# Kernel tuning notes

Hardware: AMD Instinct MI355X
Metric: run time of the kernel (lower is better)

Reference implementation:

```python
import jax, jax.numpy as jnp
import numpy as np

B, N, D, H, K = 8, 10000, 128, 4, 256
DH = D // H
M = N // 2


def make_pe(n, d):
    pos = jnp.arange(n, dtype=jnp.float32)[:, None]
    div = jnp.exp(jnp.arange(0, d, 2, dtype=jnp.float32) * (-jnp.log(10000.0) / d))
    ang = pos * div  # [n, d/2]
    pe = jnp.zeros((n, d), dtype=jnp.float32)
    pe = pe.at[:, 0::2].set(jnp.sin(ang))
    pe = pe.at[:, 1::2].set(jnp.cos(ang))
    return pe


def layernorm(z, g, b, eps=1e-5):
    mu = jnp.mean(z, -1, keepdims=True)
    var = jnp.var(z, -1, keepdims=True)
    return (z - mu) / jnp.sqrt(var + eps) * g + b


def setup_inputs():
    key = jax.random.key(0)
    ks = jax.random.split(key, 12)
    def rn(k, shape, scale):
        return jax.random.normal(k, shape, dtype=jnp.float32) * scale
    return {
        "x": rn(ks[0], (B, N), 1.0),
        "emb_w": rn(ks[1], (D, 1), 0.5),
        "emb_b": rn(ks[2], (D,), 0.02),
        "ln1_g": jnp.ones((D,), jnp.float32),
        "ln1_b": jnp.zeros((D,), jnp.float32),
        "wq": rn(ks[3], (D, D), D ** -0.5),
        "wk": rn(ks[4], (D, D), D ** -0.5),
        "wv": rn(ks[5], (D, D), D ** -0.5),
        "proj_k": rn(ks[6], (N, K), N ** -0.5),
        "proj_v": rn(ks[7], (N, K), N ** -0.5),
        "wo": rn(ks[8], (D, D), D ** -0.5),
        "wo_b": jnp.zeros((D,), jnp.float32),
        "ln2_g": jnp.ones((D,), jnp.float32),
        "ln2_b": jnp.zeros((D,), jnp.float32),
        "w1": rn(ks[9], (4 * D, D), D ** -0.5),
        "b1": jnp.zeros((4 * D,), jnp.float32),
        "w2": rn(ks[10], (D, 4 * D), (4 * D) ** -0.5),
        "b2": jnp.zeros((D,), jnp.float32),
        "fc_w": rn(ks[11], (M, N), N ** -0.5),
        "fc_b": jnp.zeros((M,), jnp.float32),
    }


def reference(x, emb_w, emb_b, ln1_g, ln1_b, wq, wk, wv, proj_k, proj_v, wo, wo_b,
              ln2_g, ln2_b, w1, b1, w2, b2, fc_w, fc_b):
    b, n = x.shape
    # Linear embedding of scalar per position: [B,N] -> [B,N,D]
    xe = x[..., None] @ emb_w.T + emb_b
    xe = xe + make_pe(n, D)
    # --- Linformer self-attention block (pre-norm + residual) ---
    hn = layernorm(xe, ln1_g, ln1_b)
    q = hn @ wq.T                                        # [B,N,D]
    k = jnp.einsum('bnd,nk->bkd', hn @ wk.T, proj_k)     # low-rank keys   [B,K,D]
    v = jnp.einsum('bnd,nk->bkd', hn @ wv.T, proj_v)     # low-rank values [B,K,D]
    q = q.reshape(b, n, H, DH).transpose(0, 2, 1, 3)     # [B,H,N,DH]
    k = k.reshape(b, K, H, DH).transpose(0, 2, 1, 3)     # [B,H,K,DH]
    v = v.reshape(b, K, H, DH).transpose(0, 2, 1, 3)
    attn = jax.nn.softmax(jnp.einsum('bhnd,bhkd->bhnk', q, k) * (DH ** -0.5), axis=-1)
    out = jnp.einsum('bhnk,bhkd->bhnd', attn, v).transpose(0, 2, 1, 3).reshape(b, n, D)
    xe = xe + out @ wo.T + wo_b
    # --- FeedForward block (pre-norm + residual, exact GELU) ---
    hn = layernorm(xe, ln2_g, ln2_b)
    xe = xe + (jax.nn.gelu(hn @ w1.T + b1, approximate=False) @ w2.T + b2)
    # fc over seq dim (Linear(N, N//2) applied to [B,D,N]) then sum-pool over D
    y = jnp.einsum('bnd,mn->bdm', xe, fc_w) + fc_b       # [B,D,M]
    return jnp.sum(y, axis=1)                            # [B,M]
```

## Files before the change

### kernel.cpp

```cpp
#include <hip/hip_runtime.h>

constexpr int B_ = 8, N_ = 10000, D_ = 128, H_ = 4, K_ = 256, M_ = 5000, DFF_ = 512;
constexpr int NPAD = 10240;

typedef __attribute__((ext_vector_type(8))) short bf16x8;
typedef __attribute__((ext_vector_type(4))) float f32x4;

__device__ __forceinline__ float bf2f(unsigned short u) {
    unsigned x = ((unsigned)u) << 16; float f; __builtin_memcpy(&f, &x, 4); return f;
}
__device__ __forceinline__ unsigned short f2bf(float f) {
    unsigned x; __builtin_memcpy(&x, &f, 4);
    x = (x + 0x7fffu + ((x >> 16) & 1u)) >> 16;
    return (unsigned short)x;
}
__device__ __forceinline__ unsigned pack2(float a, float b) {
    return (unsigned)f2bf(a) | ((unsigned)f2bf(b) << 16);
}
__device__ __forceinline__ float gelu_exact(float v) {
    return 0.5f * v * (1.0f + erff(v * 0.70710678118654752f));
}

__global__ __launch_bounds__(256) void cvt_w_k(
    const float* __restrict__ s0, const float* __restrict__ s1, const float* __restrict__ s2,
    const float* __restrict__ s3, const float* __restrict__ s4, const float* __restrict__ s5,
    unsigned short* __restrict__ d0, unsigned short* __restrict__ d1, unsigned short* __restrict__ d2,
    unsigned short* __restrict__ d3, unsigned short* __restrict__ d4, unsigned short* __restrict__ d5)
{
    const float* s; unsigned short* d; int sz;
    switch (blockIdx.y) {
        case 0: s = s0; d = d0; sz = 16384; break;
        case 1: s = s1; d = d1; sz = 16384; break;
        case 2: s = s2; d = d2; sz = 16384; break;
        case 3: s = s3; d = d3; sz = 16384; break;
        case 4: s = s4; d = d4; sz = 65536; break;
        default: s = s5; d = d5; sz = 65536; break;
    }
    const int idx = (blockIdx.x * 256 + threadIdx.x) * 8;
    if (idx >= sz) return;
    float4 a = *(const float4*)(s + idx);
    float4 b = *(const float4*)(s + idx + 4);
    uint4 p;
    p.x = pack2(a.x, a.y); p.y = pack2(a.z, a.w);
    p.z = pack2(b.x, b.y); p.w = pack2(b.z, b.w);
    *(uint4*)(d + idx) = p;
}

__global__ __launch_bounds__(256) void ptt_k(
    const float* __restrict__ pK, const float* __restrict__ pV, unsigned short* __restrict__ Pt)
{
    __shared__ __align__(16) char lds[16384];
    const int t = threadIdx.x;
    const int n0 = blockIdx.x * 64, k0 = blockIdx.y * 128, which = blockIdx.z;
    const float* P = which ? pV : pK;
    {
        const int nl = t >> 2, cc = t & 3;
        const int n = n0 + nl;
        uint4 v[4] = {};
        if (n < N_) {
            const float4* src = (const float4*)(P + (size_t)n * K_ + k0 + cc * 32);
            #pragma unroll
            for (int j = 0; j < 4; ++j) {
                float4 a = src[2 * j], b = src[2 * j + 1];
                uint4 p; p.x = pack2(a.x, a.y); p.y = pack2(a.z, a.w);
                p.z = pack2(b.x, b.y); p.w = pack2(b.z, b.w);
                v[j] = p;
            }
        }
        #pragma unroll
        for (int j = 0; j < 4; ++j) {
            int ch = (cc * 4 + j) ^ (nl & 15);
            *(uint4*)(lds + nl * 256 + ch * 16) = v[j];
        }
    }
    __syncthreads();
    {
        const int eb = t >> 3, nb = t & 7;
        unsigned short r0_[8], r1_[8], r2_[8], r3_[8];
        #pragma unroll
        for (int i = 0; i < 8; ++i) {
            int n = nb * 8 + i;
            int byte_ = n * 256 + (((eb >> 1) ^ (n & 15)) << 4) + ((eb & 1) << 3);
            uint2 dv = *(const uint2*)(lds + byte_);
            r0_[i] = (unsigned short)(dv.x & 0xffff); r1_[i] = (unsigned short)(dv.x >> 16);
            r2_[i] = (unsigned short)(dv.y & 0xffff); r3_[i] = (unsigned short)(dv.y >> 16);
        }
        size_t dbase = ((size_t)which * 256 + k0 + eb * 4) * NPAD + n0 + nb * 8;
        *(uint4*)&Pt[dbase]            = *(uint4*)r0_;
        *(uint4*)&Pt[dbase + NPAD]     = *(uint4*)r1_;
        *(uint4*)&Pt[dbase + 2 * NPAD] = *(uint4*)r2_;
        *(uint4*)&Pt[dbase + 3 * NPAD] = *(uint4*)r3_;
    }
}

__global__ __launch_bounds__(256) void hnt_k(
    const unsigned short* __restrict__ hn, unsigned short* __restrict__ hnT)
{
    __shared__ __align__(16) char lds[16384];
    const int t = threadIdx.x;
    const int n0 = blockIdx.x * 64, b = blockIdx.z;
    {
        const int nl = t >> 2, cc = t & 3;
        const int n = n0 + nl;
        uint4 v[4] = {};
        if (n < N_) {
            const uint4* src = (const uint4*)(hn + ((size_t)(b * N_ + n)) * D_ + cc * 32);
            #pragma unroll
            for (int j = 0; j < 4; ++j) v[j] = src[j];
        }
        #pragma unroll
        for (int j = 0; j < 4; ++j) {
            int ch = (cc * 4 + j) ^ (nl & 15);
            *(uint4*)(lds + nl * 256 + ch * 16) = v[j];
        }
    }
    __syncthreads();
    {
        const int eb = t >> 3, nb = t & 7;
        unsigned short r0_[8], r1_[8], r2_[8], r3_[8];
        #pragma unroll
        for (int i = 0; i < 8; ++i) {
            int n = nb * 8 + i;
            int byte_ = n * 256 + (((eb >> 1) ^ (n & 15)) << 4) + ((eb & 1) << 3);
            uint2 dv = *(const uint2*)(lds + byte_);
            r0_[i] = (unsigned short)(dv.x & 0xffff); r1_[i] = (unsigned short)(dv.x >> 16);
            r2_[i] = (unsigned short)(dv.y & 0xffff); r3_[i] = (unsigned short)(dv.y >> 16);
        }
        size_t dbase = ((size_t)b * 128 + eb * 4) * NPAD + n0 + nb * 8;
        *(uint4*)&hnT[dbase]            = *(uint4*)r0_;
        *(uint4*)&hnT[dbase + NPAD]     = *(uint4*)r1_;
        *(uint4*)&hnT[dbase + 2 * NPAD] = *(uint4*)r2_;
        *(uint4*)&hnT[dbase + 3 * NPAD] = *(uint4*)r3_;
    }
}

__global__ __launch_bounds__(256) void embed_ln_k(
    const float* __restrict__ x, const float* __restrict__ ew, const float* __restrict__ eb,
    const float* __restrict__ g, const float* __restrict__ bb,
    float* __restrict__ xe, unsigned short* __restrict__ hnb)
{
    const int r = blockIdx.x * 4 + (threadIdx.x >> 6);
    const int lane = threadIdx.x & 63;
    const int n = r % N_;
    const float xv = x[r];
    const float ang = (float)n * expf((float)lane * -0.14391156829962788f);
    float sv, cv; sincosf(ang, &sv, &cv);
    const int d0 = 2 * lane;
    float e0 = xv * ew[d0]     + eb[d0]     + sv;
    float e1 = xv * ew[d0 + 1] + eb[d0 + 1] + cv;
    float sum = e0 + e1, sq = e0 * e0 + e1 * e1;
    #pragma unroll
    for (int off = 32; off; off >>= 1) { sum += __shfl_xor(sum, off); sq += __shfl_xor(sq, off); }
    const float mu = sum * (1.f / 128.f);
    const float var = sq * (1.f / 128.f) - mu * mu;
    const float rs = rsqrtf(var + 1e-5f);
    const size_t base = (size_t)r * D_ + d0;
    float2 ev; ev.x = e0; ev.y = e1;
    *(float2*)&xe[base] = ev;
    *(unsigned*)&hnb[base] = pack2((e0 - mu) * rs * g[d0] + bb[d0],
                                   (e1 - mu) * rs * g[d0 + 1] + bb[d0 + 1]);
}

__global__ __launch_bounds__(256) void ln_k(
    const float* __restrict__ in, const float* __restrict__ g, const float* __restrict__ bb,
    unsigned short* __restrict__ outb)
{
    const int r = blockIdx.x * 4 + (threadIdx.x >> 6);
    const int lane = threadIdx.x & 63;
    const int d0 = 2 * lane;
    const size_t base = (size_t)r * D_ + d0;
    const float2 ev = *(const float2*)&in[base];
    float sum = ev.x + ev.y, sq = ev.x * ev.x + ev.y * ev.y;
    #pragma unroll
    for (int off = 32; off; off >>= 1) { sum += __shfl_xor(sum, off); sq += __shfl_xor(sq, off); }
    const float mu = sum * (1.f / 128.f);
    const float var = sq * (1.f / 128.f) - mu * mu;
    const float rs = rsqrtf(var + 1e-5f);
    *(unsigned*)&outb[base] = pack2((ev.x - mu) * rs * g[d0] + bb[d0],
                                    (ev.y - mu) * rs * g[d0 + 1] + bb[d0 + 1]);
}

enum { M_Q = 0, M_PROJ = 1, M_SMALL = 2, M_WO = 3, M_W1 = 4, M_W2 = 5 };

template<int MODE>
__global__ __launch_bounds__(256) void mgemm_k(
    const unsigned short* __restrict__ Abase, const unsigned short* __restrict__ Wbase,
    const unsigned short* __restrict__ Walt,
    const float* __restrict__ bias, float* __restrict__ Cf, unsigned short* __restrict__ Cb)
{
    constexpr int NSTEP = (MODE == M_PROJ) ? 20 : (MODE == M_W2 ? 16 : 4);
    constexpr int SA = (MODE == M_PROJ) ? NPAD : (MODE == M_W2 ? 512 : 128);
    constexpr int SB = SA;
    constexpr int NCTOT = (MODE == M_W1) ? 512 : 128;
    constexpr bool HASBIAS = (MODE == M_WO || MODE == M_W1 || MODE == M_W2);
    constexpr bool GELU = (MODE == M_W1);
    constexpr bool RES = (MODE == M_WO || MODE == M_W2);
    constexpr bool OBF = (MODE == M_Q || MODE == M_W1 || MODE == M_SMALL);

    __shared__ __align__(16) char lds[16384];

    const int t = threadIdx.x;
    const int bx = blockIdx.x, by = blockIdx.y, bz = blockIdx.z;

    const unsigned short* Ag; const unsigned short* Wg; size_t cbase;
    if (MODE == M_PROJ) {
        const int b = (bz >> 4) & 7, chunk = bz & 15, which = bz >> 7;
        Ag = Abase + (size_t)which * 256 * NPAD + (size_t)bx * 128 * NPAD + chunk * 640;
        Wg = Wbase + (size_t)b * 128 * NPAD + chunk * 640;
        cbase = (size_t)bz * 32768 + (size_t)bx * 16384;
    } else if (MODE == M_SMALL) {
        Ag = Abase + (size_t)bz * 2048 * 128 + (size_t)bx * 128 * 128;
        Wg = bz ? Walt : Wbase;
        cbase = (size_t)bz * 262144 + (size_t)bx * 16384;
    } else {
        Ag = Abase + (size_t)bx * 128 * SA;
        Wg = Wbase + (size_t)by * 128 * SB;
        cbase = (size_t)bx * 128 * NCTOT + (size_t)by * 128;
    }

    const int srow = t >> 1, hib = 2 * (t & 1);
    const unsigned short* aptr = Ag + (size_t)srow * SA + hib * 8;
    const unsigned short* wptr = Wg + (size_t)srow * SB + hib * 8;
    const int swz = (srow >> 1) & 3;
    char* la0 = lds + srow * 64 + ((hib ^ swz) << 4);
    char* la1 = lds + srow * 64 + (((hib + 1) ^ swz) << 4);
    char* lw0 = la0 + 8192;
    char* lw1 = la1 + 8192;

    const int w = t >> 6, l = t & 63;
    const int wrow = (w & 1) * 64, wcol = (w >> 1) * 64;
    int offA[4], offW[4];
    #pragma unroll
    for (int mi = 0; mi < 4; ++mi) {
        int ra = wrow + mi * 16 + (l & 15);
        offA[mi] = ra * 64 + (((l >> 4) ^ ((ra >> 1) & 3)) << 4);
        int rw = wcol + mi * 16 + (l & 15);
        offW[mi] = 8192 + rw * 64 + (((l >> 4) ^ ((rw >> 1) & 3)) << 4);
    }

    f32x4 acc[4][4] = {};

    for (int s = 0; s < NSTEP; ++s) {
        uint4 va0 = *(const uint4*)(aptr);
        uint4 va1 = *(const uint4*)(aptr + 8);
        uint4 vw0 = *(const uint4*)(wptr);
        uint4 vw1 = *(const uint4*)(wptr + 8);
        aptr += 32; wptr += 32;
        __syncthreads();
        *(uint4*)la0 = va0; *(uint4*)la1 = va1;
        *(uint4*)lw0 = vw0; *(uint4*)lw1 = vw1;
        __syncthreads();
        bf16x8 af[4], bfr[4];
        #pragma unroll
        for (int mi = 0; mi < 4; ++mi) {
            af[mi] = *(const bf16x8*)(lds + offA[mi]);
            bfr[mi] = *(const bf16x8*)(lds + offW[mi]);
        }
        #pragma unroll
        for (int mi = 0; mi < 4; ++mi)
            #pragma unroll
            for (int ni = 0; ni < 4; ++ni)
                acc[mi][ni] = __builtin_amdgcn_mfma_f32_16x16x32_bf16(af[mi], bfr[ni], acc[mi][ni], 0, 0, 0);
    }

    const int lrb = wrow + ((l >> 4) << 2);
    const int lcb = wcol + (l & 15);
    #pragma unroll
    for (int mi = 0; mi < 4; ++mi) {
        #pragma unroll
        for (int ni = 0; ni < 4; ++ni) {
            const int lc = lcb + ni * 16;
            #pragma unroll
            for (int r = 0; r < 4; ++r) {
                const int lr = lrb + mi * 16 + r;
                float v = acc[mi][ni][r];
                if (HASBIAS) v += bias[by * 128 + lc];
                if (GELU) v = gelu_exact(v);
                const size_t ci = cbase + (size_t)lr * NCTOT + lc;
                if (RES) v += Cf[ci];
                if (OBF) Cb[ci] = f2bf(v); else Cf[ci] = v;
            }
        }
    }
}

__global__ __launch_bounds__(256) void reduce_k(
    const float* __restrict__ partials, unsigned short* __restrict__ lowKV)
{
    const int gid = blockIdx.x * 256 + threadIdx.x;
    const int wb = gid >> 15, r = gid & 32767;
    const float* p = partials + (size_t)wb * 16 * 32768 + r;
    float s = 0.f;
    #pragma unroll
    for (int c = 0; c < 16; ++c) s += p[c * 32768];
    lowKV[gid] = f2bf(s);
}

__global__ __launch_bounds__(256) void attn_mfma_k(
    const unsigned short* __restrict__ q, const unsigned short* __restrict__ kv,
    unsigned short* __restrict__ outp)
{
    __shared__ __align__(16) char lds[65536];
    const int t = threadIdx.x;
    const int w = t >> 6, l = t & 63;
    const int g = l >> 4, ql = l & 15;
    const int h = blockIdx.y, b = blockIdx.z;
    const int q0 = blockIdx.x * 256;
    const float SC = 0.17677669529663687f;

    #pragma unroll
    for (int i = 0; i < 4; ++i) {
        const int r = (t >> 2) + 64 * i;
        const uint4 v = *(const uint4*)(kv + ((size_t)(b * 256 + r) * 128 + h * 32) + (t & 3) * 8);
        *(uint4*)(lds + r * 64 + (((t & 3) * 16) ^ ((r & 3) << 4))) = v;
    }
    {
        const int kp = t & 127, dhalf = t >> 7;
        const unsigned short* vsrc = kv + 262144 + ((size_t)(b * 256 + 2 * kp) * 128 + h * 32 + 16 * dhalf);
        uint4 a0 = *(const uint4*)(vsrc);
        uint4 a1 = *(const uint4*)(vsrc + 8);
        uint4 c0 = *(const uint4*)(vsrc + 128);
        uint4 c1 = *(const uint4*)(vsrc + 136);
        const unsigned short* pa0 = (const unsigned short*)&a0;
        const unsigned short* pa1 = (const unsigned short*)&a1;
        const unsigned short* pc0 = (const unsigned short*)&c0;
        const unsigned short* pc1 = (const unsigned short*)&c1;
        #pragma unroll
        for (int j = 0; j < 8; ++j) {
            const int row = 16 * dhalf + j;
            unsigned u = (unsigned)pa0[j] | ((unsigned)pc0[j] << 16);
            *(unsigned*)(lds + 16384 + row * 512 + ((4 * kp) ^ ((row & 7) << 4))) = u;
        }
        #pragma unroll
        for (int j = 0; j < 8; ++j) {
            const int row = 16 * dhalf + 8 + j;
            unsigned u = (unsigned)pa1[j] | ((unsigned)pc1[j] << 16);
            *(unsigned*)(lds + 16384 + row * 512 + ((4 * kp) ^ ((row & 7) << 4))) = u;
        }
    }
    bf16x8 qfr[4];
    #pragma unroll
    for (int qf = 0; qf < 4; ++qf) {
        int n = q0 + w * 64 + qf * 16 + ql;
        if (n >= N_) n = N_ - 1;
        qfr[qf] = *(const bf16x8*)(q + ((size_t)(b * N_ + n) * 128 + h * 32 + g * 8));
    }
    __syncthreads();

    char* Pw = lds + 32768 + w * 8192;
    f32x4 oacc[2][4] = {};
    float m_run[4], l_run[4];
    #pragma unroll
    for (int qf = 0; qf < 4; ++qf) { m_run[qf] = -1e30f; l_run[qf] = 0.f; }

    for (int kt = 0; kt < 4; ++kt) {
        const int kb = kt * 64;
        bf16x8 kfr[4];
        #pragma unroll
        for (int kf = 0; kf < 4; ++kf) {
            const int r = kb + kf * 16 + ql;
            kfr[kf] = *(const bf16x8*)(lds + r * 64 + ((g * 16) ^ ((r & 3) << 4)));
        }
        f32x4 s_[4][4];
        #pragma unroll
        for (int kf = 0; kf < 4; ++kf)
            #pragma unroll
            for (int qf = 0; qf < 4; ++qf) {
                f32x4 z = {0.f, 0.f, 0.f, 0.f};
                s_[kf][qf] = __builtin_amdgcn_mfma_f32_16x16x32_bf16(kfr[kf], qfr[qf], z, 0, 0, 0);
            }
        #pragma unroll
        for (int qf = 0; qf < 4; ++qf) {
            float mx = -1e30f;
            #pragma unroll
            for (int kf = 0; kf < 4; ++kf)
                #pragma unroll
                for (int r = 0; r < 4; ++r) mx = fmaxf(mx, s_[kf][qf][r]);
            mx = fmaxf(mx, __shfl_xor(mx, 16));
            mx = fmaxf(mx, __shfl_xor(mx, 32));
            mx *= SC;
            const float mnew = fmaxf(m_run[qf], mx);
            const float corr = __expf(m_run[qf] - mnew);
            m_run[qf] = mnew;
            l_run[qf] *= corr;
            #pragma unroll
            for (int df = 0; df < 2; ++df) {
                oacc[df][qf][0] *= corr; oacc[df][qf][1] *= corr;
                oacc[df][qf][2] *= corr; oacc[df][qf][3] *= corr;
            }
            float p_[4][4]; float ssum = 0.f;
            #pragma unroll
            for (int kf = 0; kf < 4; ++kf)
                #pragma unroll
                for (int r = 0; r < 4; ++r) {
                    const float pv = __expf(s_[kf][qf][r] * SC - mnew);
                    p_[kf][r] = pv; ssum += pv;
                }
            ssum += __shfl_xor(ssum, 16);
            ssum += __shfl_xor(ssum, 32);
            l_run[qf] += ssum;
            const int qrow = qf * 16 + ql;
            #pragma unroll
            for (int kf = 0; kf < 4; ++kf) {
                uint2 pk;
                pk.x = pack2(p_[kf][0], p_[kf][1]);
                pk.y = pack2(p_[kf][2], p_[kf][3]);
                *(uint2*)(Pw + qrow * 128 + ((kf * 32 + g * 8) ^ ((qrow & 7) << 4))) = pk;
            }
        }
        asm volatile("s_waitcnt lgkmcnt(0)" ::: "memory");
        __builtin_amdgcn_sched_barrier(0);
        #pragma unroll
        for (int ks = 0; ks < 2; ++ks) {
            bf16x8 vt_[2];
            #pragma unroll
            for (int df = 0; df < 2; ++df) {
                const int row = df * 16 + ql;
                vt_[df] = *(const bf16x8*)(lds + 16384 + row * 512 +
                           ((kb * 2 + ks * 64 + g * 16) ^ ((row & 7) << 4)));
            }
            #pragma unroll
            for (int qf = 0; qf < 4; ++qf) {
                const int qrow = qf * 16 + ql;
                bf16x8 pf = *(const bf16x8*)(Pw + qrow * 128 + ((ks * 64 + g * 16) ^ ((qrow & 7) << 4)));
                #pragma unroll
                for (int df = 0; df < 2; ++df)
                    oacc[df][qf] = __builtin_amdgcn_mfma_f32_16x16x32_bf16(vt_[df], pf, oacc[df][qf], 0, 0, 0);
            }
        }
        asm volatile("s_waitcnt lgkmcnt(0)" ::: "memory");
        __builtin_amdgcn_sched_barrier(0);
    }

    float inv_[4];
    #pragma unroll
    for (int qf = 0; qf < 4; ++qf) inv_[qf] = 1.f / l_run[qf];
    #pragma unroll
    for (int qf = 0; qf < 4; ++qf) {
        const int qrow = qf * 16 + ql;
        #pragma unroll
        for (int df = 0; df < 2; ++df) {
            const unsigned lo = pack2(oacc[df][qf][0] * inv_[qf], oacc[df][qf][1] * inv_[qf]);
            const unsigned hi = pack2(oacc[df][qf][2] * inv_[qf], oacc[df][qf][3] * inv_[qf]);
            *(unsigned*)(Pw + qrow * 64 + ((df * 32 + g * 8) ^ ((qrow & 3) << 4))) = lo;
            *(unsigned*)(Pw + qrow * 64 + ((df * 32 + g * 8 + 4) ^ ((qrow & 3) << 4))) = hi;
        }
    }
    asm volatile("s_waitcnt lgkmcnt(0)" ::: "memory");
    __builtin_amdgcn_sched_barrier(0);
    #pragma unroll
    for (int pp = 0; pp < 4; ++pp) {
        const int qrow = pp * 16 + (l >> 2), c = l & 3;
        const uint4 v = *(const uint4*)(Pw + qrow * 64 + ((c * 16) ^ ((qrow & 3) << 4)));
        const int n = q0 + w * 64 + qrow;
        if (n < N_)
            *(uint4*)(outp + ((size_t)(b * N_ + n) * 128 + h * 32 + c * 8)) = v;
    }
}

__global__ __launch_bounds__(256) void rowsum_k(const float* __restrict__ xe, float* __restrict__ st)
{
    const int r = blockIdx.x * 4 + (threadIdx.x >> 6);
    const int lane = threadIdx.x & 63;
    const float2 v = *(const float2*)&xe[(size_t)r * D_ + 2 * lane];
    float sum = v.x + v.y;
    #pragma unroll
    for (int off = 32; off; off >>= 1) sum += __shfl_xor(sum, off);
    if (lane == 0) {
        const int b = r / N_, n = r % N_;
        st[(size_t)n * 8 + b] = sum;
    }
}

__global__ __launch_bounds__(256) void fc_k(
    const float* __restrict__ st, const float* __restrict__ fcw, const float* __restrict__ fcb,
    float* __restrict__ out)
{
    __shared__ float wred[4][4][8];
    const int t = threadIdx.x;
    const int m0 = blockIdx.x * 4;
    float acc[4][8] = {};
    for (int n = t; n < N_; n += 256) {
        const float4 sa = *(const float4*)&st[(size_t)n * 8];
        const float4 sb = *(const float4*)&st[(size_t)n * 8 + 4];
        #pragma unroll
        for (int mm = 0; mm < 4; ++mm) {
            const float w = fcw[(size_t)(m0 + mm) * N_ + n];
            acc[mm][0] = fmaf(w, sa.x, acc[mm][0]); acc[mm][1] = fmaf(w, sa.y, acc[mm][1]);
            acc[mm][2] = fmaf(w, sa.z, acc[mm][2]); acc[mm][3] = fmaf(w, sa.w, acc[mm][3]);
            acc[mm][4] = fmaf(w, sb.x, acc[mm][4]); acc[mm][5] = fmaf(w, sb.y, acc[mm][5]);
            acc[mm][6] = fmaf(w, sb.z, acc[mm][6]); acc[mm][7] = fmaf(w, sb.w, acc[mm][7]);
        }
    }
    #pragma unroll
    for (int mm = 0; mm < 4; ++mm)
        #pragma unroll
        for (int bb = 0; bb < 8; ++bb) {
            float v = acc[mm][bb];
            #pragma unroll
            for (int off = 32; off; off >>= 1) v += __shfl_xor(v, off);
            acc[mm][bb] = v;
        }
    const int lane = t & 63, wv_ = t >> 6;
    if (lane == 0)
        #pragma unroll
        for (int mm = 0; mm < 4; ++mm)
            #pragma unroll
            for (int bb = 0; bb < 8; ++bb) wred[wv_][mm][bb] = acc[mm][bb];
    __syncthreads();
    if (t < 32) {
        const int mm = t >> 3, bb = t & 7;
        float v = wred[0][mm][bb] + wred[1][mm][bb] + wred[2][mm][bb] + wred[3][mm][bb];
        out[(size_t)bb * M_ + m0 + mm] = v + 128.f * fcb[m0 + mm];
    }
}

extern "C" void kernel_launch(void* const* d_in, const int* in_sizes, int n_in,
                              void* d_out, int out_size, void* d_ws, size_t ws_size,
                              hipStream_t stream)
{
    const float* x      = (const float*)d_in[0];
    const float* emb_w  = (const float*)d_in[1];
    const float* emb_b  = (const float*)d_in[2];
    const float* ln1_g  = (const float*)d_in[3];
    const float* ln1_b  = (const float*)d_in[4];
    const float* wq     = (const float*)d_in[5];
    const float* wk     = (const float*)d_in[6];
    const float* wv     = (const float*)d_in[7];
    const float* projk  = (const float*)d_in[8];
    const float* projv  = (const float*)d_in[9];
    const float* wo     = (const float*)d_in[10];
    const float* wo_b   = (const float*)d_in[11];
    const float* ln2_g  = (const float*)d_in[12];
    const float* ln2_b  = (const float*)d_in[13];
    const float* w1     = (const float*)d_in[14];
    const float* b1     = (const float*)d_in[15];
    const float* w2     = (const float*)d_in[16];
    const float* b2     = (const float*)d_in[17];
    const float* fcw    = (const float*)d_in[18];
    const float* fcb    = (const float*)d_in[19];
    float* out = (float*)d_out;

    char* W = (char*)d_ws;
    float*          xe       = (float*)W;
    unsigned short* hnb      = (unsigned short*)(W + 40960000);
    char*           region   = W + 61440000;
    unsigned short* qb       = (unsigned short*)region;
    unsigned short* hnT      = (unsigned short*)(region + 20480000);
    unsigned short* Pt       = (unsigned short*)(region + 41451520);
    float*          partials = (float*)(region + 51937280);
    unsigned short* hid      = (unsigned short*)region;
    unsigned short* lowKV    = (unsigned short*)(W + 146931712);
    unsigned short* klowb    = (unsigned short*)(W + 147980288);
    unsigned short* wqb      = (unsigned short*)(W + 150077440);
    unsigned short* wkb      = wqb + 16384;
    unsigned short* wvb      = wkb + 16384;
    unsigned short* wob      = wvb + 16384;
    unsigned short* w1b      = wob + 16384;
    unsigned short* w2b      = w1b + 65536;
    float*          st       = (float*)(W + 150470656);

    const size_t BN = (size_t)B_ * N_;

    cvt_w_k<<<dim3(32, 6), 256, 0, stream>>>(wq, wk, wv, wo, w1, w2, wqb, wkb, wvb, wob, w1b, w2b);
    ptt_k<<<dim3(160, 2, 2), 256, 0, stream>>>(projk, projv, Pt);
    embed_ln_k<<<BN / 4, 256, 0, stream>>>(x, emb_w, emb_b, ln1_g, ln1_b, xe, hnb);
    hnt_k<<<dim3(160, 1, 8), 256, 0, stream>>>(hnb, hnT);
    mgemm_k<M_Q><<<dim3(625, 1, 1), 256, 0, stream>>>(hnb, wqb, nullptr, nullptr, nullptr, qb);
    mgemm_k<M_PROJ><<<dim3(2, 1, 256), 256, 0, stream>>>(Pt, hnT, nullptr, nullptr, partials, nullptr);
    reduce_k<<<2048, 256, 0, stream>>>(partials, lowKV);
    mgemm_k<M_SMALL><<<dim3(16, 1, 2), 256, 0, stream>>>(lowKV, wkb, wvb, nullptr, nullptr, klowb);
    attn_mfma_k<<<dim3(40, H_, B_), 256, 0, stream>>>(qb, klowb, hnb);
    mgemm_k<M_WO><<<dim3(625, 1, 1), 256, 0, stream>>>(hnb, wob, nullptr, wo_b, xe, nullptr);
    ln_k<<<BN / 4, 256, 0, stream>>>(xe, ln2_g, ln2_b, hnb);
    mgemm_k<M_W1><<<dim3(625, 4, 1), 256, 0, stream>>>(hnb, w1b, nullptr, b1, nullptr, hid);
    mgemm_k<M_W2><<<dim3(625, 1, 1), 256, 0, stream>>>(hid, w2b, nullptr, b2, xe, nullptr);
    rowsum_k<<<BN / 4, 256, 0, stream>>>(xe, st);
    fc_k<<<M_ / 4, 256, 0, stream>>>(st, fcw, fcb, out);
}
```

Baseline: 344.1 us.

## Fuse LN2 and row-sum into GEMM epilogues, store residual in bf16

The second layernorm moves into the WO GEMM epilogue and the final row-sum into the W2 GEMM epilogue, using cross-wave row reductions through LDS. This removes the standalone ln_k and rowsum_k kernels. The residual stream is now stored as bf16 instead of fp32, which cuts its memory traffic but lowers its precision. The projection GEMM split-K is halved to 8 chunks, and the attention online softmax now rescales only when the running max increases.

```diff
diff --git a/kernel.cpp b/kernel.cpp
--- a/kernel.cpp
+++ b/kernel.cpp
@@ -137,7 +137,7 @@
 __global__ __launch_bounds__(256) void embed_ln_k(
     const float* __restrict__ x, const float* __restrict__ ew, const float* __restrict__ eb,
     const float* __restrict__ g, const float* __restrict__ bb,
-    float* __restrict__ xe, unsigned short* __restrict__ hnb)
+    unsigned short* __restrict__ xeb, unsigned short* __restrict__ hnb)
 {
     const int r = blockIdx.x * 4 + (threadIdx.x >> 6);
     const int lane = threadIdx.x & 63;
@@ -155,29 +155,9 @@
     const float var = sq * (1.f / 128.f) - mu * mu;
     const float rs = rsqrtf(var + 1e-5f);
     const size_t base = (size_t)r * D_ + d0;
-    float2 ev; ev.x = e0; ev.y = e1;
-    *(float2*)&xe[base] = ev;
+    *(unsigned*)&xeb[base] = pack2(e0, e1);
     *(unsigned*)&hnb[base] = pack2((e0 - mu) * rs * g[d0] + bb[d0],
                                    (e1 - mu) * rs * g[d0 + 1] + bb[d0 + 1]);
-}
-
-__global__ __launch_bounds__(256) void ln_k(
-    const float* __restrict__ in, const float* __restrict__ g, const float* __restrict__ bb,
-    unsigned short* __restrict__ outb)
-{
-    const int r = blockIdx.x * 4 + (threadIdx.x >> 6);
-    const int lane = threadIdx.x & 63;
-    const int d0 = 2 * lane;
-    const size_t base = (size_t)r * D_ + d0;
-    const float2 ev = *(const float2*)&in[base];
-    float sum = ev.x + ev.y, sq = ev.x * ev.x + ev.y * ev.y;
-    #pragma unroll
-    for (int off = 32; off; off >>= 1) { sum += __shfl_xor(sum, off); sq += __shfl_xor(sq, off); }
-    const float mu = sum * (1.f / 128.f);
-    const float var = sq * (1.f / 128.f) - mu * mu;
-    const float rs = rsqrtf(var + 1e-5f);
-    *(unsigned*)&outb[base] = pack2((ev.x - mu) * rs * g[d0] + bb[d0],
-                                    (ev.y - mu) * rs * g[d0 + 1] + bb[d0 + 1]);
 }
 
 enum { M_Q = 0, M_PROJ = 1, M_SMALL = 2, M_WO = 3, M_W1 = 4, M_W2 = 5 };
@@ -186,16 +166,16 @@
 __global__ __launch_bounds__(256) void mgemm_k(
     const unsigned short* __restrict__ Abase, const unsigned short* __restrict__ Wbase,
     const unsigned short* __restrict__ Walt,
-    const float* __restrict__ bias, float* __restrict__ Cf, unsigned short* __restrict__ Cb)
-{
-    constexpr int NSTEP = (MODE == M_PROJ) ? 20 : (MODE == M_W2 ? 16 : 4);
+    const float* __restrict__ bias, float* __restrict__ Cf, unsigned short* __restrict__ Cb,
+    const unsigned short* __restrict__ xebr, unsigned short* __restrict__ xebw,
+    const float* __restrict__ lng, const float* __restrict__ lnb, float* __restrict__ st)
+{
+    constexpr int NSTEP = (MODE == M_PROJ) ? 40 : (MODE == M_W2 ? 16 : 4);
     constexpr int SA = (MODE == M_PROJ) ? NPAD : (MODE == M_W2 ? 512 : 128);
     constexpr int SB = SA;
     constexpr int NCTOT = (MODE == M_W1) ? 512 : 128;
-    constexpr bool HASBIAS = (MODE == M_WO || MODE == M_W1 || MODE == M_W2);
     constexpr bool GELU = (MODE == M_W1);
-    constexpr bool RES = (MODE == M_WO || MODE == M_W2);
-    constexpr bool OBF = (MODE == M_Q || MODE == M_W1 || MODE == M_SMALL);
+    constexpr bool FUSED = (MODE == M_WO || MODE == M_W2);
 
     __shared__ __align__(16) char lds[16384];
 
@@ -204,9 +184,9 @@
 
     const unsigned short* Ag; const unsigned short* Wg; size_t cbase;
     if (MODE == M_PROJ) {
-        const int b = (bz >> 4) & 7, chunk = bz & 15, which = bz >> 7;
-        Ag = Abase + (size_t)which * 256 * NPAD + (size_t)bx * 128 * NPAD + chunk * 640;
-        Wg = Wbase + (size_t)b * 128 * NPAD + chunk * 640;
+        const int b = (bz >> 3) & 7, chunk = bz & 7, which = bz >> 6;
+        Ag = Abase + (size_t)which * 256 * NPAD + (size_t)bx * 128 * NPAD + chunk * 1280;
+        Wg = Wbase + (size_t)b * 128 * NPAD + chunk * 1280;
         cbase = (size_t)bz * 32768 + (size_t)bx * 16384;
     } else if (MODE == M_SMALL) {
         Ag = Abase + (size_t)bz * 2048 * 128 + (size_t)bx * 128 * 128;
@@ -228,6 +208,7 @@
     char* lw1 = la1 + 8192;
 
     const int w = t >> 6, l = t & 63;
+    const int g = l >> 4;
     const int wrow = (w & 1) * 64, wcol = (w >> 1) * 64;
     int offA[4], offW[4];
     #pragma unroll
@@ -263,8 +244,94 @@
                 acc[mi][ni] = __builtin_amdgcn_mfma_f32_16x16x32_bf16(af[mi], bfr[ni], acc[mi][ni], 0, 0, 0);
     }
 
-    const int lrb = wrow + ((l >> 4) << 2);
+    const int lrb = wrow + (g << 2);
     const int lcb = wcol + (l & 15);
+
+    if (FUSED) {
+        float rsum[4][4], rsq[4][4];
+        #pragma unroll
+        for (int mi = 0; mi < 4; ++mi)
+            #pragma unroll
+            for (int r = 0; r < 4; ++r) { rsum[mi][r] = 0.f; rsq[mi][r] = 0.f; }
+        #pragma unroll
+        for (int mi = 0; mi < 4; ++mi)
+            #pragma unroll
+            for (int ni = 0; ni < 4; ++ni) {
+                const int lc = lcb + ni * 16;
+                #pragma unroll
+                for (int r = 0; r < 4; ++r) {
+                    const int lr = lrb + mi * 16 + r;
+                    const size_t ci = cbase + (size_t)lr * 128 + lc;
+                    float v = acc[mi][ni][r] + bias[lc] + bf2f(xebr[ci]);
+                    acc[mi][ni][r] = v;
+                    rsum[mi][r] += v;
+                    if (MODE == M_WO) rsq[mi][r] += v * v;
+                }
+            }
+        #pragma unroll
+        for (int mi = 0; mi < 4; ++mi)
+            #pragma unroll
+            for (int r = 0; r < 4; ++r) {
+                float s_ = rsum[mi][r], q_ = rsq[mi][r];
+                #pragma unroll
+                for (int off = 1; off < 16; off <<= 1) {
+                    s_ += __shfl_xor(s_, off);
+                    if (MODE == M_WO) q_ += __shfl_xor(q_, off);
+                }
+                rsum[mi][r] = s_; rsq[mi][r] = q_;
+            }
+        __syncthreads();
+        float2* red = (float2*)lds;
+        if ((l & 15) == 0) {
+            #pragma unroll
+            for (int mi = 0; mi < 4; ++mi)
+                #pragma unroll
+                for (int r = 0; r < 4; ++r) {
+                    const int lr = lrb + mi * 16 + r;
+                    float2 e; e.x = rsum[mi][r]; e.y = rsq[mi][r];
+                    red[(w >> 1) * 128 + lr] = e;
+                }
+        }
+        __syncthreads();
+        if (MODE == M_WO) {
+            #pragma unroll
+            for (int mi = 0; mi < 4; ++mi)
+                #pragma unroll
+                for (int r = 0; r < 4; ++r) {
+                    const int lr = lrb + mi * 16 + r;
+                    const float2 e0 = red[lr], e1 = red[128 + lr];
+                    const float mu = (e0.x + e1.x) * (1.f / 128.f);
+                    const float var = (e0.y + e1.y) * (1.f / 128.f) - mu * mu;
+                    const float rstd = rsqrtf(var + 1e-5f);
+                    #pragma unroll
+                    for (int ni = 0; ni < 4; ++ni) {
+                        const int lc = lcb + ni * 16;
+                        const size_t ci = cbase + (size_t)lr * 128 + lc;
+                        const float xv = acc[mi][ni][r];
+                        xebw[ci] = f2bf(xv);
+                        Cb[ci] = f2bf((xv - mu) * rstd * lng[lc] + lnb[lc]);
+                    }
+                }
+        } else {
+            if ((l & 15) == 0 && (w >> 1) == 0) {
+                #pragma unroll
+                for (int mi = 0; mi < 4; ++mi)
+                    #pragma unroll
+                    for (int r = 0; r < 4; ++r) {
+                        const int lr = lrb + mi * 16 + r;
+                        const float total = red[lr].x + red[128 + lr].x;
+                        const int grow = bx * 128 + lr;
+                        const int bidx = grow / N_;
+                        const int n = grow - bidx * N_;
+                        st[(size_t)n * 8 + bidx] = total;
+                    }
+            }
+        }
+        return;
+    }
+
+    constexpr bool HASBIAS = (MODE == M_W1);
+    constexpr bool OBF = (MODE == M_Q || MODE == M_W1 || MODE == M_SMALL);
     #pragma unroll
     for (int mi = 0; mi < 4; ++mi) {
         #pragma unroll
@@ -277,7 +344,6 @@
                 if (HASBIAS) v += bias[by * 128 + lc];
                 if (GELU) v = gelu_exact(v);
                 const size_t ci = cbase + (size_t)lr * NCTOT + lc;
-                if (RES) v += Cf[ci];
                 if (OBF) Cb[ci] = f2bf(v); else Cf[ci] = v;
             }
         }
@@ -289,10 +355,10 @@
 {
     const int gid = blockIdx.x * 256 + threadIdx.x;
     const int wb = gid >> 15, r = gid & 32767;
-    const float* p = partials + (size_t)wb * 16 * 32768 + r;
+    const float* p = partials + (size_t)wb * 8 * 32768 + r;
     float s = 0.f;
     #pragma unroll
-    for (int c = 0; c < 16; ++c) s += p[c * 32768];
+    for (int c = 0; c < 8; ++c) s += p[c * 32768];
     lowKV[gid] = f2bf(s);
 }
 
@@ -379,21 +445,22 @@
             mx = fmaxf(mx, __shfl_xor(mx, 16));
             mx = fmaxf(mx, __shfl_xor(mx, 32));
             mx *= SC;
-            const float mnew = fmaxf(m_run[qf], mx);
-            const float corr = __expf(m_run[qf] - mnew);
-            m_run[qf] = mnew;
-            l_run[qf] *= corr;
-            #pragma unroll
-            for (int df = 0; df < 2; ++df) {
-                oacc[df][qf][0] *= corr; oacc[df][qf][1] *= corr;
-                oacc[df][qf][2] *= corr; oacc[df][qf][3] *= corr;
+            if (mx > m_run[qf]) {
+                const float corr = __expf(m_run[qf] - mx);
+                l_run[qf] *= corr;
+                #pragma unroll
+                for (int df = 0; df < 2; ++df) {
+                    oacc[df][qf][0] *= corr; oacc[df][qf][1] *= corr;
+                    oacc[df][qf][2] *= corr; oacc[df][qf][3] *= corr;
+                }
+                m_run[qf] = mx;
             }
             float p_[4][4]; float ssum = 0.f;
             #pragma unroll
             for (int kf = 0; kf < 4; ++kf)
                 #pragma unroll
                 for (int r = 0; r < 4; ++r) {
-                    const float pv = __expf(s_[kf][qf][r] * SC - mnew);
+                    const float pv = __expf(s_[kf][qf][r] * SC - m_run[qf]);
                     p_[kf][r] = pv; ssum += pv;
                 }
             ssum += __shfl_xor(ssum, 16);
@@ -455,20 +522,6 @@
         const int n = q0 + w * 64 + qrow;
         if (n < N_)
             *(uint4*)(outp + ((size_t)(b * N_ + n) * 128 + h * 32 + c * 8)) = v;
-    }
-}
-
-__global__ __launch_bounds__(256) void rowsum_k(const float* __restrict__ xe, float* __restrict__ st)
-{
-    const int r = blockIdx.x * 4 + (threadIdx.x >> 6);
-    const int lane = threadIdx.x & 63;
-    const float2 v = *(const float2*)&xe[(size_t)r * D_ + 2 * lane];
-    float sum = v.x + v.y;
-    #pragma unroll
-    for (int off = 32; off; off >>= 1) sum += __shfl_xor(sum, off);
-    if (lane == 0) {
-        const int b = r / N_, n = r % N_;
-        st[(size_t)n * 8 + b] = sum;
     }
 }
 
@@ -542,7 +595,7 @@
     float* out = (float*)d_out;
 
     char* W = (char*)d_ws;
-    float*          xe       = (float*)W;
+    unsigned short* xeb      = (unsigned short*)W;
     unsigned short* hnb      = (unsigned short*)(W + 40960000);
     char*           region   = W + 61440000;
     unsigned short* qb       = (unsigned short*)region;
@@ -564,17 +617,21 @@
 
     cvt_w_k<<<dim3(32, 6), 256, 0, stream>>>(wq, wk, wv, wo, w1, w2, wqb, wkb, wvb, wob, w1b, w2b);
     ptt_k<<<dim3(160, 2, 2), 256, 0, stream>>>(projk, projv, Pt);
-    embed_ln_k<<<BN / 4, 256, 0, stream>>>(x, emb_w, emb_b, ln1_g, ln1_b, xe, hnb);
+    embed_ln_k<<<BN / 4, 256, 0, stream>>>(x, emb_w, emb_b, ln1_g, ln1_b, xeb, hnb);
     hnt_k<<<dim3(160, 1, 8), 256, 0, stream>>>(hnb, hnT);
-    mgemm_k<M_Q><<<dim3(625, 1, 1), 256, 0, stream>>>(hnb, wqb, nullptr, nullptr, nullptr, qb);
-    mgemm_k<M_PROJ><<<dim3(2, 1, 256), 256, 0, stream>>>(Pt, hnT, nullptr, nullptr, partials, nullptr);
+    mgemm_k<M_Q><<<dim3(625, 1, 1), 256, 0, stream>>>(hnb, wqb, nullptr, nullptr, nullptr, qb,
+                                                      nullptr, nullptr, nullptr, nullptr, nullptr);
+    mgemm_k<M_PROJ><<<dim3(2, 1, 128), 256, 0, stream>>>(Pt, hnT, nullptr, nullptr, partials, nullptr,
+                                                         nullptr, nullptr, nullptr, nullptr, nullptr);
     reduce_k<<<2048, 256, 0, stream>>>(partials, lowKV);
-    mgemm_k<M_SMALL><<<dim3(16, 1, 2), 256, 0, stream>>>(lowKV, wkb, wvb, nullptr, nullptr, klowb);
+    mgemm_k<M_SMALL><<<dim3(16, 1, 2), 256, 0, stream>>>(lowKV, wkb, wvb, nullptr, nullptr, klowb,
+                                                         nullptr, nullptr, nullptr, nullptr, nullptr);
     attn_mfma_k<<<dim3(40, H_, B_), 256, 0, stream>>>(qb, klowb, hnb);
-    mgemm_k<M_WO><<<dim3(625, 1, 1), 256, 0, stream>>>(hnb, wob, nullptr, wo_b, xe, nullptr);
-    ln_k<<<BN / 4, 256, 0, stream>>>(xe, ln2_g, ln2_b, hnb);
-    mgemm_k<M_W1><<<dim3(625, 4, 1), 256, 0, stream>>>(hnb, w1b, nullptr, b1, nullptr, hid);
-    mgemm_k<M_W2><<<dim3(625, 1, 1), 256, 0, stream>>>(hid, w2b, nullptr, b2, xe, nullptr);
-    rowsum_k<<<BN / 4, 256, 0, stream>>>(xe, st);
+    mgemm_k<M_WO><<<dim3(625, 1, 1), 256, 0, stream>>>(hnb, wob, nullptr, wo_b, nullptr, hnb,
+                                                       xeb, xeb, ln2_g, ln2_b, nullptr);
+    mgemm_k<M_W1><<<dim3(625, 4, 1), 256, 0, stream>>>(hnb, w1b, nullptr, b1, nullptr, hid,
+                                                       nullptr, nullptr, nullptr, nullptr, nullptr);
+    mgemm_k<M_W2><<<dim3(625, 1, 1), 256, 0, stream>>>(hid, w2b, nullptr, b2, nullptr, nullptr,
+                                                       xeb, nullptr, nullptr, nullptr, st);
     fc_k<<<M_ / 4, 256, 0, stream>>>(st, fcw, fcb, out);
 }
```

New measurement: 328.8 us. 4.5% less time.
